# Kernel tuning notes

Hardware: AMD Instinct MI355X
Metric: run time of the kernel (lower is better)

The kernel has to match this reference:

```python
import jax, jax.numpy as jnp
import numpy as np
import math

B, S, D = 2, 2048, 2048
H = 16
DK = D // H


def build_rotary(dim, seq_len):
    inv_freq = 1.0 / (10000.0 ** (np.arange(0, dim, 2, dtype=np.float32) / dim))
    t = np.arange(seq_len, dtype=np.float32)
    freqs = np.einsum('i,j->ij', t, inv_freq)
    emb = np.concatenate([freqs, freqs], axis=-1)  # [S, dim]
    return jnp.asarray(np.cos(emb))[None, None], jnp.asarray(np.sin(emb))[None, None]


def rotate_half(x):
    x1, x2 = jnp.split(x, 2, axis=-1)
    return jnp.concatenate([-x2, x1], axis=-1)


def setup_inputs() -> dict:
    key = jax.random.key(0)
    ks = jax.random.split(key, 12)
    s = 1.0 / math.sqrt(D)
    inp = {
        'query': jax.random.normal(ks[0], (B, S, D), jnp.float32),
        'key': jax.random.normal(ks[1], (B, S, D), jnp.float32),
        'value': jax.random.normal(ks[2], (B, S, D), jnp.float32),
        'mask': jnp.tril(jnp.ones((S, S), bool))[None, None],  # causal [1,1,S,S]
        'wq': jax.random.uniform(ks[3], (D, D), jnp.float32, -s, s),
        'bq': jax.random.uniform(ks[4], (D,), jnp.float32, -s, s),
        'wk': jax.random.uniform(ks[5], (D, D), jnp.float32, -s, s),
        'bk': jax.random.uniform(ks[6], (D,), jnp.float32, -s, s),
        'wv': jax.random.uniform(ks[7], (D, D), jnp.float32, -s, s),
        'bv': jax.random.uniform(ks[8], (D,), jnp.float32, -s, s),
        'wo': jax.random.uniform(ks[9], (D, D), jnp.float32, -s, s),
        'bo': jax.random.uniform(ks[10], (D,), jnp.float32, -s, s),
    }
    return inp


def reference(query, key, value, mask, wq, bq, wk, bk, wv, bv, wo, bo):
    Bc, Sc, _ = query.shape
    # QKV projections -> [B, H, S, DK]
    def proj(x, w, b):
        return (x @ w.T + b).reshape(Bc, Sc, H, DK).transpose(0, 2, 1, 3)
    q = proj(query, wq, bq)
    k = proj(key, wk, bk)
    v = proj(value, wv, bv)
    # inline RoPE
    cos, sin = build_rotary(DK, Sc)
    cos = cos.astype(query.dtype)
    sin = sin.astype(query.dtype)
    q = q * cos + rotate_half(q) * sin
    k = k * cos + rotate_half(k) * sin
    # attention (dropout in eval / identity)
    scores = jnp.einsum('bhqd,bhkd->bhqk', q, k) / math.sqrt(DK)
    scores = jnp.where(mask, scores.astype(jnp.float32), -1e9)
    p = jax.nn.softmax(scores, axis=-1)
    x = jnp.einsum('bhqk,bhkd->bhqd', p, v)
    x = x.transpose(0, 2, 1, 3).reshape(Bc, Sc, H * DK)
    return x @ wo.T + bo
```

## Files before the change

### kernel.cpp

```cpp
#include <hip/hip_runtime.h>
#include <hip/hip_bf16.h>

#define Bc 2
#define Sc 2048
#define Dc 2048
#define Hc 16
#define DKc 128
#define Mc (Bc * Sc)
#define Kc Dc
#define Nc Dc
#define NX ((size_t)Bc * Sc * Dc)
#define NW ((size_t)Dc * Dc)

#define SM_C 0.1275174366f

typedef unsigned short u16;
using bf16x8  = __bf16 __attribute__((ext_vector_type(8)));
using ushort8 = unsigned short __attribute__((ext_vector_type(8)));
using ushort4v = unsigned short __attribute__((ext_vector_type(4)));
using floatx4 = float __attribute__((ext_vector_type(4)));
using float4v = float __attribute__((ext_vector_type(4)));

__device__ __forceinline__ u16 f2bf(float f) {
  union { float f; unsigned u; } x; x.f = f;
  unsigned r = x.u + 0x7fffu + ((x.u >> 16) & 1u);
  return (u16)(r >> 16);
}
__device__ __forceinline__ float bf2f(u16 u) {
  union { unsigned u; float f; } x; x.u = ((unsigned)u) << 16;
  return x.f;
}
__device__ __forceinline__ bf16x8 load8(const u16* p) {
  return __builtin_bit_cast(bf16x8, *(const ushort8*)p);
}
__device__ __forceinline__ floatx4 mfma16(bf16x8 a, bf16x8 b, floatx4 c) {
  return __builtin_amdgcn_mfma_f32_16x16x32_bf16(a, b, c, 0, 0, 0);
}
__device__ __forceinline__ void async16(const void* g, void* l) {
  __builtin_amdgcn_global_load_lds(
      (__attribute__((address_space(1))) void*)(g),
      (__attribute__((address_space(3))) void*)(l), 16, 0, 0);
}

__global__ __launch_bounds__(256) void cast_all(
    const float* __restrict__ q, const float* __restrict__ k,
    const float* __restrict__ v, const float* __restrict__ wq,
    const float* __restrict__ wk, const float* __restrict__ wv,
    const float* __restrict__ wo, u16* __restrict__ dst) {
  size_t i4 = (size_t)blockIdx.x * 256 + threadIdx.x;
  size_t e = i4 * 4;
  const float* src; size_t off;
  if (e < 3 * NX) {
    size_t w = e / NX;
    src = (w == 0) ? q : (w == 1) ? k : v;
    off = e - w * NX;
  } else {
    size_t e2 = e - 3 * NX;
    size_t w = e2 / NW;
    src = (w == 0) ? wq : (w == 1) ? wk : (w == 2) ? wv : wo;
    off = e2 - w * NW;
  }
  float4v val = *(const float4v*)(src + off);
  ushort4v o;
  o.x = f2bf(val.x); o.y = f2bf(val.y); o.z = f2bf(val.z); o.w = f2bf(val.w);
  *(ushort4v*)(dst + e) = o;
}

__device__ __forceinline__ void gemm_body(
    const u16* __restrict__ A, const u16* __restrict__ W,
    const float* __restrict__ bias, u16* __restrict__ out_bf,
    float* __restrict__ out_f, int epi, int m0, int n0, u16* Asl, u16* Bsl) {
  const int tid = threadIdx.x;
  const int wid = tid >> 6, lane = tid & 63;
  const int l15 = lane & 15, quad = lane >> 4;
  const int wm = wid & 1, wn = wid >> 1;

  floatx4 acc[4][4] = {};
  const int row_s = tid >> 2;
  const int col_s = (tid & 3) * 8;

  for (int k0 = 0; k0 < Kc; k0 += 32) {
    __syncthreads();
    const u16* ga0 = A + (size_t)(m0 + row_s) * Kc + k0 + col_s;
    const u16* gb0 = W + (size_t)(n0 + row_s) * Kc + k0 + col_s;
    async16(ga0, &Asl[tid * 8]);
    async16(ga0 + (size_t)64 * Kc, &Asl[2048 + tid * 8]);
    async16(gb0, &Bsl[tid * 8]);
    async16(gb0 + (size_t)64 * Kc, &Bsl[2048 + tid * 8]);
    __syncthreads();
    bf16x8 af[4], bfr[4];
#pragma unroll
    for (int i = 0; i < 4; i++)
      af[i] = load8(&Asl[(wm * 64 + i * 16 + l15) * 32 + quad * 8]);
#pragma unroll
    for (int j = 0; j < 4; j++)
      bfr[j] = load8(&Bsl[(wn * 64 + j * 16 + l15) * 32 + quad * 8]);
#pragma unroll
    for (int i = 0; i < 4; i++)
#pragma unroll
      for (int j = 0; j < 4; j++)
        acc[i][j] = mfma16(af[i], bfr[j], acc[i][j]);
  }

#pragma unroll
  for (int j = 0; j < 4; j++) {
    int col = n0 + wn * 64 + j * 16 + l15;
    float bv = bias[col];
#pragma unroll
    for (int i = 0; i < 4; i++) {
      int rowb = m0 + wm * 64 + i * 16 + quad * 4;
#pragma unroll
      for (int r = 0; r < 4; r++) {
        float v = acc[i][j][r] + bv;
        int row = rowb + r;
        if (epi == 2) {
          out_f[(size_t)row * Nc + col] = v;
        } else {
          int b = row >> 11, s = row & 2047;
          int h = col >> 7, dk = col & 127;
          size_t addr = (epi == 0)
              ? ((size_t)(b * Hc + h) * Sc + s) * DKc + dk
              : ((size_t)(b * Hc + h) * DKc + dk) * Sc + s;
          out_bf[addr] = f2bf(v);
        }
      }
    }
  }
}

__global__ __launch_bounds__(256, 2) void gemm_qkv(
    const u16* __restrict__ xq, const u16* __restrict__ xk,
    const u16* __restrict__ xv, const u16* __restrict__ wcat,
    const float* __restrict__ bq, const float* __restrict__ bk,
    const float* __restrict__ bv, u16* __restrict__ qhw,
    u16* __restrict__ khw, u16* __restrict__ vtw) {
  __shared__ u16 Asl[128 * 32];
  __shared__ u16 Bsl[128 * 32];
  const int proj = blockIdx.x >> 4;
  const int n0 = (blockIdx.x & 15) * 128;
  const int m0 = blockIdx.y * 128;
  const u16* A = (proj == 0) ? xq : (proj == 1) ? xk : xv;
  const u16* W = wcat + (size_t)proj * 2048 * Kc;
  const float* bias = (proj == 0) ? bq : (proj == 1) ? bk : bv;
  u16* outp = (proj == 0) ? qhw : (proj == 1) ? khw : vtw;
  gemm_body(A, W, bias, outp, nullptr, (proj == 2) ? 1 : 0, m0, n0, Asl, Bsl);
}

__global__ __launch_bounds__(256, 2) void gemm_out(
    const u16* __restrict__ A, const u16* __restrict__ W,
    const float* __restrict__ bias, float* __restrict__ out_f) {
  __shared__ u16 Asl[128 * 32];
  __shared__ u16 Bsl[128 * 32];
  gemm_body(A, W, bias, nullptr, out_f, 2, blockIdx.y * 128, blockIdx.x * 128,
            Asl, Bsl);
}

__global__ __launch_bounds__(256) void rope_kernel(u16* __restrict__ q,
                                                   u16* __restrict__ k) {
  int i = blockIdx.x * 256 + threadIdx.x;
  int d = i & 63;
  int s = (i >> 6) & (Sc - 1);
  int bh = i >> 17;
  size_t base = ((size_t)bh * Sc + s) * DKc;
  float inv_freq = exp2f((float)d * (-13.287712379549449f / 64.0f));
  float ang = (float)s * inv_freq;
  float sn, cs;
  sincosf(ang, &sn, &cs);
  float q1 = bf2f(q[base + d]), q2 = bf2f(q[base + d + 64]);
  q[base + d]      = f2bf((q1 * cs - q2 * sn) * SM_C);
  q[base + d + 64] = f2bf((q2 * cs + q1 * sn) * SM_C);
  float k1 = bf2f(k[base + d]), k2 = bf2f(k[base + d + 64]);
  k[base + d]      = f2bf(k1 * cs - k2 * sn);
  k[base + d + 64] = f2bf(k2 * cs + k1 * sn);
}

__global__ __launch_bounds__(256) void attn_kernel(
    const u16* __restrict__ qh, const u16* __restrict__ kh,
    const u16* __restrict__ vt, u16* __restrict__ ao) {
  __shared__ u16 Ksl[128 * 128];
  __shared__ u16 Vsl[144 * 128];
  const int tid = threadIdx.x;
  const int wid = tid >> 6, lane = tid & 63;
  const int l15 = lane & 15, quad = lane >> 4;
  const int qt = (blockIdx.z == 0) ? 15 - (int)blockIdx.x : (int)blockIdx.x;
  const int h = blockIdx.y, bb = blockIdx.z;
  const int bh = bb * Hc + h;
  const int q0 = qt * 128;
  const u16* qbase = qh + (size_t)bh * Sc * DKc;
  const u16* kbase = kh + (size_t)bh * Sc * DKc;
  const u16* vbase = vt + (size_t)bh * DKc * Sc;

  const int srow = tid >> 4;
  const int scol = (tid & 15) * 8;
  const int sdst = ((tid & 15) ^ srow) * 8;

  {
    int r = 128 + srow;
    u16 val = (r == 128) ? (u16)0x3F80 : (u16)0;
#pragma unroll
    for (int j = 0; j < 8; j++) Vsl[r * 128 + scol + j] = val;
  }

  bf16x8 qf[2][4];
#pragma unroll
  for (int mt = 0; mt < 2; mt++)
#pragma unroll
    for (int kq = 0; kq < 4; kq++)
      qf[mt][kq] = load8(qbase + (size_t)(q0 + wid * 32 + mt * 16 + l15) * DKc +
                         kq * 32 + quad * 8);

  floatx4 accO[2][9] = {};

  ushort8 kr[8], vr[8];
#pragma unroll
  for (int c = 0; c < 8; c++) {
    int rr = c * 16 + srow;
    kr[c] = *(const ushort8*)(kbase + (size_t)rr * DKc + scol);
    vr[c] = *(const ushort8*)(vbase + (size_t)rr * Sc + scol);
  }

  for (int kt = 0; kt <= qt; kt++) {
    __syncthreads();
#pragma unroll
    for (int c = 0; c < 8; c++) {
      int rr = c * 16 + srow;
      *(ushort8*)&Ksl[rr * 128 + sdst] = kr[c];
      *(ushort8*)&Vsl[rr * 128 + sdst] = vr[c];
    }
    __syncthreads();

    floatx4 sacc[2][8] = {};
#pragma unroll
    for (int kk = 0; kk < 4; kk++) {
      const int sb = ((kk * 4 + quad) ^ l15) * 8;
#pragma unroll
      for (int nt = 0; nt < 8; nt++) {
        bf16x8 kf = load8(&Ksl[(nt * 16 + l15) * 128 + sb]);
        sacc[0][nt] = mfma16(qf[0][kk], kf, sacc[0][nt]);
        sacc[1][nt] = mfma16(qf[1][kk], kf, sacc[1][nt]);
      }
    }

    if (kt == qt) {
#pragma unroll
      for (int nt = 0; nt < 8; nt++) {
        int kcol = nt * 16 + l15;
#pragma unroll
        for (int mt = 0; mt < 2; mt++) {
          int qrow = wid * 32 + mt * 16 + quad * 4;
#pragma unroll
          for (int r = 0; r < 4; r++)
            if (kcol > qrow + r) sacc[mt][nt][r] = -1e30f;
        }
      }
    }

#pragma unroll
    for (int mt = 0; mt < 2; mt++)
#pragma unroll
      for (int nt = 0; nt < 8; nt++)
#pragma unroll
        for (int r = 0; r < 4; r++)
          sacc[mt][nt][r] = exp2f(sacc[mt][nt][r]);

    __syncthreads();

    u16* Pw = &Ksl[wid * 4096];
#pragma unroll
    for (int mt = 0; mt < 2; mt++)
#pragma unroll
      for (int nt = 0; nt < 8; nt++)
#pragma unroll
        for (int r = 0; r < 4; r++) {
          int row = mt * 16 + quad * 4 + r;
          int col = nt * 16 + l15;
          int sb = (col >> 3) ^ (row & 15);
          Pw[row * 128 + sb * 8 + (col & 7)] = f2bf(sacc[mt][nt][r]);
        }

    if (kt < qt) {
      const u16* kb = kbase + (size_t)(kt + 1) * 128 * DKc;
#pragma unroll
      for (int c = 0; c < 8; c++) {
        int rr = c * 16 + srow;
        kr[c] = *(const ushort8*)(kb + (size_t)rr * DKc + scol);
        vr[c] = *(const ushort8*)(vbase + (size_t)rr * Sc + (kt + 1) * 128 + scol);
      }
    }

#pragma unroll
    for (int kk = 0; kk < 4; kk++) {
      const int sb = ((kk * 4 + quad) ^ l15) * 8;
      bf16x8 pf0 = load8(&Pw[(0 * 16 + l15) * 128 + sb]);
      bf16x8 pf1 = load8(&Pw[(1 * 16 + l15) * 128 + sb]);
#pragma unroll
      for (int nt = 0; nt < 9; nt++) {
        bf16x8 vf = load8(&Vsl[(nt * 16 + l15) * 128 + sb]);
        accO[0][nt] = mfma16(pf0, vf, accO[0][nt]);
        accO[1][nt] = mfma16(pf1, vf, accO[1][nt]);
      }
    }
  }

#pragma unroll
  for (int mt = 0; mt < 2; mt++)
#pragma unroll
    for (int r = 0; r < 4; r++) {
      float lsum = __shfl(accO[mt][8][r], lane & 48);
      float inv = 1.0f / lsum;
      int gq = q0 + wid * 32 + mt * 16 + quad * 4 + r;
      size_t rowbase = ((size_t)bb * Sc + gq) * Dc + h * DKc;
#pragma unroll
      for (int nt = 0; nt < 8; nt++)
        ao[rowbase + nt * 16 + l15] = f2bf(accO[mt][nt][r] * inv);
    }
}

extern "C" void kernel_launch(void* const* d_in, const int* in_sizes, int n_in,
                              void* d_out, int out_size, void* d_ws,
                              size_t ws_size, hipStream_t stream) {
  const float* q  = (const float*)d_in[0];
  const float* k  = (const float*)d_in[1];
  const float* v  = (const float*)d_in[2];
  const float* wq = (const float*)d_in[4];
  const float* bq = (const float*)d_in[5];
  const float* wk = (const float*)d_in[6];
  const float* bk = (const float*)d_in[7];
  const float* wv = (const float*)d_in[8];
  const float* bv = (const float*)d_in[9];
  const float* wo = (const float*)d_in[10];
  const float* bo = (const float*)d_in[11];
  float* out = (float*)d_out;

  u16* ws = (u16*)d_ws;
  u16* xq  = ws;
  u16* xk  = ws + NX;
  u16* xv  = ws + 2 * NX;
  u16* wcat = ws + 3 * NX;
  u16* wob = ws + 3 * NX + 3 * NW;
  u16* qhw = ws + 3 * NX + 4 * NW;
  u16* khw = ws + 4 * NX + 4 * NW;
  u16* vtw = ws + 5 * NX + 4 * NW;
  u16* aow = ws + 6 * NX + 4 * NW;

  {
    size_t tot4 = (3 * NX + 4 * NW) / 4;
    cast_all<<<dim3((unsigned)(tot4 / 256)), 256, 0, stream>>>(
        q, k, v, wq, wk, wv, wo, ws);
  }
  gemm_qkv<<<dim3(48, Mc / 128), 256, 0, stream>>>(
      xq, xk, xv, wcat, bq, bk, bv, qhw, khw, vtw);
  rope_kernel<<<dim3(Bc * Hc * Sc * 64 / 256), 256, 0, stream>>>(qhw, khw);
  attn_kernel<<<dim3(Sc / 128, Hc, Bc), 256, 0, stream>>>(qhw, khw, vtw, aow);
  gemm_out<<<dim3(Nc / 128, Mc / 128), 256, 0, stream>>>(aow, wob, bo, out);
}
```

Baseline: 533.2 us.

## Rewrite projection GEMMs as 256x256 tiles with 4-stage async LDS pipeline

```diff
diff --git a/kernel.cpp b/kernel.cpp
--- a/kernel.cpp
+++ b/kernel.cpp
@@ -11,6 +11,7 @@
 #define Nc Dc
 #define NX ((size_t)Bc * Sc * Dc)
 #define NW ((size_t)Dc * Dc)
+#define NTK (Kc / 32)
 
 #define SM_C 0.1275174366f
 
@@ -66,52 +67,96 @@
   *(ushort4v*)(dst + e) = o;
 }
 
-__device__ __forceinline__ void gemm_body(
+__device__ __forceinline__ void gemm256_body(
     const u16* __restrict__ A, const u16* __restrict__ W,
     const float* __restrict__ bias, u16* __restrict__ out_bf,
-    float* __restrict__ out_f, int epi, int m0, int n0, u16* Asl, u16* Bsl) {
+    float* __restrict__ out_f, int epi, int m0, int n0,
+    u16* __restrict__ lds ) {
   const int tid = threadIdx.x;
   const int wid = tid >> 6, lane = tid & 63;
   const int l15 = lane & 15, quad = lane >> 4;
-  const int wm = wid & 1, wn = wid >> 1;
-
-  floatx4 acc[4][4] = {};
-  const int row_s = tid >> 2;
-  const int col_s = (tid & 3) * 8;
-
-  for (int k0 = 0; k0 < Kc; k0 += 32) {
-    __syncthreads();
-    const u16* ga0 = A + (size_t)(m0 + row_s) * Kc + k0 + col_s;
-    const u16* gb0 = W + (size_t)(n0 + row_s) * Kc + k0 + col_s;
-    async16(ga0, &Asl[tid * 8]);
-    async16(ga0 + (size_t)64 * Kc, &Asl[2048 + tid * 8]);
-    async16(gb0, &Bsl[tid * 8]);
-    async16(gb0 + (size_t)64 * Kc, &Bsl[2048 + tid * 8]);
-    __syncthreads();
-    bf16x8 af[4], bfr[4];
-#pragma unroll
-    for (int i = 0; i < 4; i++)
-      af[i] = load8(&Asl[(wm * 64 + i * 16 + l15) * 32 + quad * 8]);
-#pragma unroll
-    for (int j = 0; j < 4; j++)
-      bfr[j] = load8(&Bsl[(wn * 64 + j * 16 + l15) * 32 + quad * 8]);
-#pragma unroll
-    for (int i = 0; i < 4; i++)
-#pragma unroll
-      for (int j = 0; j < 4; j++)
-        acc[i][j] = mfma16(af[i], bfr[j], acc[i][j]);
-  }
-
-#pragma unroll
-  for (int j = 0; j < 4; j++) {
-    int col = n0 + wn * 64 + j * 16 + l15;
+  const int wm = wid >> 2, wn = wid & 3;
+
+  const int sr = tid >> 2;
+  const int sc = (((tid & 3) ^ ((tid >> 3) & 3))) * 8;
+  const u16* gA = A + (size_t)(m0 + sr) * Kc + sc;
+  const u16* gB = W + (size_t)(n0 + sr) * Kc + sc;
+  const size_t rowskip = (size_t)128 * Kc;
+
+  const int slot8 = (quad ^ ((l15 >> 1) & 3)) * 8;
+  const int arow0 = (wm * 128 + l15) * 32 + slot8;
+  const int brow0 = (wn * 64 + l15) * 32 + slot8;
+
+  floatx4 acc[8][4] = {};
+
+#pragma unroll
+  for (int t = 0; t < 3; ++t) {
+    u16* buf = lds + t * 16384;
+    async16(gA + t * 32,           buf + tid * 8);
+    async16(gA + t * 32 + rowskip, buf + 4096 + tid * 8);
+    async16(gB + t * 32,           buf + 8192 + tid * 8);
+    async16(gB + t * 32 + rowskip, buf + 12288 + tid * 8);
+  }
+  asm volatile("s_waitcnt vmcnt(8)" ::: "memory");
+  __builtin_amdgcn_s_barrier();
+
+  for (int t = 0; t < NTK; ++t) {
+    u16* buf  = lds + (t & 3) * 16384;
+    u16* nbuf = lds + ((t + 3) & 3) * 16384;
+    const bool pf = (t + 3 < NTK);
+
+    if (pf) {
+      async16(gA + (t + 3) * 32,           nbuf + tid * 8);
+      async16(gA + (t + 3) * 32 + rowskip, nbuf + 4096 + tid * 8);
+    }
+    bf16x8 bfrag[4], afrag[4];
+#pragma unroll
+    for (int n = 0; n < 4; ++n)
+      bfrag[n] = load8(buf + 8192 + brow0 + n * 512);
+#pragma unroll
+    for (int m = 0; m < 4; ++m)
+      afrag[m] = load8(buf + arow0 + m * 512);
+    __builtin_amdgcn_s_barrier();
+    __builtin_amdgcn_s_setprio(1);
+#pragma unroll
+    for (int m = 0; m < 4; ++m)
+#pragma unroll
+      for (int n = 0; n < 4; ++n)
+        acc[m][n] = mfma16(afrag[m], bfrag[n], acc[m][n]);
+    __builtin_amdgcn_s_setprio(0);
+    __builtin_amdgcn_s_barrier();
+
+    if (pf) {
+      async16(gB + (t + 3) * 32,           nbuf + 8192 + tid * 8);
+      async16(gB + (t + 3) * 32 + rowskip, nbuf + 12288 + tid * 8);
+    }
+#pragma unroll
+    for (int m = 0; m < 4; ++m)
+      afrag[m] = load8(buf + arow0 + 2048 + m * 512);
+    __builtin_amdgcn_s_barrier();
+    __builtin_amdgcn_s_setprio(1);
+#pragma unroll
+    for (int m = 0; m < 4; ++m)
+#pragma unroll
+      for (int n = 0; n < 4; ++n)
+        acc[4 + m][n] = mfma16(afrag[m], bfrag[n], acc[4 + m][n]);
+    __builtin_amdgcn_s_setprio(0);
+    if (t < NTK - 3)       asm volatile("s_waitcnt vmcnt(8)" ::: "memory");
+    else if (t == NTK - 3) asm volatile("s_waitcnt vmcnt(4)" ::: "memory");
+    else                   asm volatile("s_waitcnt vmcnt(0)" ::: "memory");
+    __builtin_amdgcn_s_barrier();
+  }
+
+#pragma unroll
+  for (int n = 0; n < 4; ++n) {
+    int col = n0 + wn * 64 + n * 16 + l15;
     float bv = bias[col];
 #pragma unroll
-    for (int i = 0; i < 4; i++) {
-      int rowb = m0 + wm * 64 + i * 16 + quad * 4;
-#pragma unroll
-      for (int r = 0; r < 4; r++) {
-        float v = acc[i][j][r] + bv;
+    for (int mi = 0; mi < 8; ++mi) {
+      int rowb = m0 + wm * 128 + mi * 16 + quad * 4;
+#pragma unroll
+      for (int r = 0; r < 4; ++r) {
+        float v = acc[mi][n][r] + bv;
         int row = rowb + r;
         if (epi == 2) {
           out_f[(size_t)row * Nc + col] = v;
@@ -128,31 +173,29 @@
   }
 }
 
-__global__ __launch_bounds__(256, 2) void gemm_qkv(
+__global__ __launch_bounds__(512, 2) void gemm_qkv256(
     const u16* __restrict__ xq, const u16* __restrict__ xk,
     const u16* __restrict__ xv, const u16* __restrict__ wcat,
     const float* __restrict__ bq, const float* __restrict__ bk,
     const float* __restrict__ bv, u16* __restrict__ qhw,
     u16* __restrict__ khw, u16* __restrict__ vtw) {
-  __shared__ u16 Asl[128 * 32];
-  __shared__ u16 Bsl[128 * 32];
-  const int proj = blockIdx.x >> 4;
-  const int n0 = (blockIdx.x & 15) * 128;
-  const int m0 = blockIdx.y * 128;
+  __shared__ u16 lds[4 * 16384];
+  const int proj = blockIdx.z;
+  const int n0 = blockIdx.x * 256;
+  const int m0 = blockIdx.y * 256;
   const u16* A = (proj == 0) ? xq : (proj == 1) ? xk : xv;
   const u16* W = wcat + (size_t)proj * 2048 * Kc;
   const float* bias = (proj == 0) ? bq : (proj == 1) ? bk : bv;
   u16* outp = (proj == 0) ? qhw : (proj == 1) ? khw : vtw;
-  gemm_body(A, W, bias, outp, nullptr, (proj == 2) ? 1 : 0, m0, n0, Asl, Bsl);
-}
-
-__global__ __launch_bounds__(256, 2) void gemm_out(
+  gemm256_body(A, W, bias, outp, nullptr, (proj == 2) ? 1 : 0, m0, n0, lds);
+}
+
+__global__ __launch_bounds__(512, 2) void gemm_out256(
     const u16* __restrict__ A, const u16* __restrict__ W,
     const float* __restrict__ bias, float* __restrict__ out_f) {
-  __shared__ u16 Asl[128 * 32];
-  __shared__ u16 Bsl[128 * 32];
-  gemm_body(A, W, bias, nullptr, out_f, 2, blockIdx.y * 128, blockIdx.x * 128,
-            Asl, Bsl);
+  __shared__ u16 lds[4 * 16384];
+  gemm256_body(A, W, bias, nullptr, out_f, 2, blockIdx.y * 256,
+               blockIdx.x * 256, lds);
 }
 
 __global__ __launch_bounds__(256) void rope_kernel(u16* __restrict__ q,
@@ -348,9 +391,9 @@
     cast_all<<<dim3((unsigned)(tot4 / 256)), 256, 0, stream>>>(
         q, k, v, wq, wk, wv, wo, ws);
   }
-  gemm_qkv<<<dim3(48, Mc / 128), 256, 0, stream>>>(
+  gemm_qkv256<<<dim3(Nc / 256, Mc / 256, 3), 512, 0, stream>>>(
       xq, xk, xv, wcat, bq, bk, bv, qhw, khw, vtw);
   rope_kernel<<<dim3(Bc * Hc * Sc * 64 / 256), 256, 0, stream>>>(qhw, khw);
   attn_kernel<<<dim3(Sc / 128, Hc, Bc), 256, 0, stream>>>(qhw, khw, vtw, aow);
-  gemm_out<<<dim3(Nc / 128, Mc / 128), 256, 0, stream>>>(aow, wob, bo, out);
-}
+  gemm_out256<<<dim3(Nc / 256, Mc / 256), 512, 0, stream>>>(aow, wob, bo, out);
+}
```

Result: slower. 557.1 us (+4.5%).

## Triple-buffer GEMM LDS tiles with async prefetch and XOR swizzle

Applied to the files above, without the earlier changes.

```diff
diff --git a/kernel.cpp b/kernel.cpp
--- a/kernel.cpp
+++ b/kernel.cpp
@@ -11,6 +11,7 @@
 #define Nc Dc
 #define NX ((size_t)Bc * Sc * Dc)
 #define NW ((size_t)Dc * Dc)
+#define NTK (Kc / 32)
 
 #define SM_C 0.1275174366f
 
@@ -69,49 +70,83 @@
 __device__ __forceinline__ void gemm_body(
     const u16* __restrict__ A, const u16* __restrict__ W,
     const float* __restrict__ bias, u16* __restrict__ out_bf,
-    float* __restrict__ out_f, int epi, int m0, int n0, u16* Asl, u16* Bsl) {
+    float* __restrict__ out_f, int epi, int m0, int n0,
+    u16* __restrict__ lds ) {
   const int tid = threadIdx.x;
   const int wid = tid >> 6, lane = tid & 63;
   const int l15 = lane & 15, quad = lane >> 4;
-  const int wm = wid & 1, wn = wid >> 1;
+  const int wm = wid >> 1, wn = wid & 1;
+
+  const int sr = tid >> 2;
+  const int sc = ((tid & 3) ^ ((tid >> 3) & 3)) * 8;
+  const u16* gA = A + (size_t)(m0 + sr) * Kc + sc;
+  const u16* gB = W + (size_t)(n0 + sr) * Kc + sc;
+  const size_t half = (size_t)64 * Kc;
+
+  const int slot8 = (quad ^ ((l15 >> 1) & 3)) * 8;
+  const int arow0 = (wm * 64 + l15) * 32 + slot8;
+  const int brow0 = 4096 + (wn * 64 + l15) * 32 + slot8;
 
   floatx4 acc[4][4] = {};
-  const int row_s = tid >> 2;
-  const int col_s = (tid & 3) * 8;
-
-  for (int k0 = 0; k0 < Kc; k0 += 32) {
-    __syncthreads();
-    const u16* ga0 = A + (size_t)(m0 + row_s) * Kc + k0 + col_s;
-    const u16* gb0 = W + (size_t)(n0 + row_s) * Kc + k0 + col_s;
-    async16(ga0, &Asl[tid * 8]);
-    async16(ga0 + (size_t)64 * Kc, &Asl[2048 + tid * 8]);
-    async16(gb0, &Bsl[tid * 8]);
-    async16(gb0 + (size_t)64 * Kc, &Bsl[2048 + tid * 8]);
-    __syncthreads();
+
+  u16* b0 = lds;
+  u16* b1 = lds + 8192;
+  u16* b2 = lds + 16384;
+
+  async16(gA,             b0 + tid * 8);
+  async16(gA + half,      b0 + 2048 + tid * 8);
+  async16(gB,             b0 + 4096 + tid * 8);
+  async16(gB + half,      b0 + 6144 + tid * 8);
+  async16(gA + 32,        b1 + tid * 8);
+  async16(gA + 32 + half, b1 + 2048 + tid * 8);
+  async16(gB + 32,        b1 + 4096 + tid * 8);
+  async16(gB + 32 + half, b1 + 6144 + tid * 8);
+  asm volatile("s_waitcnt vmcnt(4)" ::: "memory");
+  __builtin_amdgcn_s_barrier();
+
+  const u16* gAt = gA + 64;
+  const u16* gBt = gB + 64;
+
+  for (int t = 0; t < NTK; ++t) {
+    if (t < NTK - 2) {
+      async16(gAt,        b2 + tid * 8);
+      async16(gAt + half, b2 + 2048 + tid * 8);
+      async16(gBt,        b2 + 4096 + tid * 8);
+      async16(gBt + half, b2 + 6144 + tid * 8);
+    }
+
     bf16x8 af[4], bfr[4];
 #pragma unroll
-    for (int i = 0; i < 4; i++)
-      af[i] = load8(&Asl[(wm * 64 + i * 16 + l15) * 32 + quad * 8]);
-#pragma unroll
-    for (int j = 0; j < 4; j++)
-      bfr[j] = load8(&Bsl[(wn * 64 + j * 16 + l15) * 32 + quad * 8]);
-#pragma unroll
-    for (int i = 0; i < 4; i++)
-#pragma unroll
-      for (int j = 0; j < 4; j++)
-        acc[i][j] = mfma16(af[i], bfr[j], acc[i][j]);
-  }
-
-#pragma unroll
-  for (int j = 0; j < 4; j++) {
-    int col = n0 + wn * 64 + j * 16 + l15;
+    for (int m = 0; m < 4; ++m) af[m] = load8(b0 + arow0 + m * 512);
+#pragma unroll
+    for (int n = 0; n < 4; ++n) bfr[n] = load8(b0 + brow0 + n * 512);
+
+    __builtin_amdgcn_s_setprio(1);
+#pragma unroll
+    for (int m = 0; m < 4; ++m)
+#pragma unroll
+      for (int n = 0; n < 4; ++n)
+        acc[m][n] = mfma16(af[m], bfr[n], acc[m][n]);
+    __builtin_amdgcn_s_setprio(0);
+
+    if (t < NTK - 2)       asm volatile("s_waitcnt vmcnt(4)" ::: "memory");
+    else if (t == NTK - 2) asm volatile("s_waitcnt vmcnt(0)" ::: "memory");
+    __builtin_amdgcn_s_barrier();
+
+    u16* tmp = b0; b0 = b1; b1 = b2; b2 = tmp;
+    gAt += 32; gBt += 32;
+  }
+
+#pragma unroll
+  for (int n = 0; n < 4; ++n) {
+    int col = n0 + wn * 64 + n * 16 + l15;
     float bv = bias[col];
 #pragma unroll
-    for (int i = 0; i < 4; i++) {
-      int rowb = m0 + wm * 64 + i * 16 + quad * 4;
-#pragma unroll
-      for (int r = 0; r < 4; r++) {
-        float v = acc[i][j][r] + bv;
+    for (int m = 0; m < 4; ++m) {
+      int rowb = m0 + wm * 64 + m * 16 + quad * 4;
+#pragma unroll
+      for (int r = 0; r < 4; ++r) {
+        float v = acc[m][n][r] + bv;
         int row = rowb + r;
         if (epi == 2) {
           out_f[(size_t)row * Nc + col] = v;
@@ -128,31 +163,29 @@
   }
 }
 
-__global__ __launch_bounds__(256, 2) void gemm_qkv(
+__global__ __launch_bounds__(256, 3) void gemm_qkv(
     const u16* __restrict__ xq, const u16* __restrict__ xk,
     const u16* __restrict__ xv, const u16* __restrict__ wcat,
     const float* __restrict__ bq, const float* __restrict__ bk,
     const float* __restrict__ bv, u16* __restrict__ qhw,
     u16* __restrict__ khw, u16* __restrict__ vtw) {
-  __shared__ u16 Asl[128 * 32];
-  __shared__ u16 Bsl[128 * 32];
-  const int proj = blockIdx.x >> 4;
-  const int n0 = (blockIdx.x & 15) * 128;
+  __shared__ u16 lds[3 * 8192];
+  const int proj = blockIdx.z;
+  const int n0 = blockIdx.x * 128;
   const int m0 = blockIdx.y * 128;
   const u16* A = (proj == 0) ? xq : (proj == 1) ? xk : xv;
   const u16* W = wcat + (size_t)proj * 2048 * Kc;
   const float* bias = (proj == 0) ? bq : (proj == 1) ? bk : bv;
   u16* outp = (proj == 0) ? qhw : (proj == 1) ? khw : vtw;
-  gemm_body(A, W, bias, outp, nullptr, (proj == 2) ? 1 : 0, m0, n0, Asl, Bsl);
-}
-
-__global__ __launch_bounds__(256, 2) void gemm_out(
+  gemm_body(A, W, bias, outp, nullptr, (proj == 2) ? 1 : 0, m0, n0, lds);
+}
+
+__global__ __launch_bounds__(256, 3) void gemm_out(
     const u16* __restrict__ A, const u16* __restrict__ W,
     const float* __restrict__ bias, float* __restrict__ out_f) {
-  __shared__ u16 Asl[128 * 32];
-  __shared__ u16 Bsl[128 * 32];
-  gemm_body(A, W, bias, nullptr, out_f, 2, blockIdx.y * 128, blockIdx.x * 128,
-            Asl, Bsl);
+  __shared__ u16 lds[3 * 8192];
+  gemm_body(A, W, bias, nullptr, out_f, 2, blockIdx.y * 128,
+            blockIdx.x * 128, lds);
 }
 
 __global__ __launch_bounds__(256) void rope_kernel(u16* __restrict__ q,
@@ -348,7 +381,7 @@
     cast_all<<<dim3((unsigned)(tot4 / 256)), 256, 0, stream>>>(
         q, k, v, wq, wk, wv, wo, ws);
   }
-  gemm_qkv<<<dim3(48, Mc / 128), 256, 0, stream>>>(
+  gemm_qkv<<<dim3(Nc / 128, Mc / 128, 3), 256, 0, stream>>>(
       xq, xk, xv, wcat, bq, bk, bv, qhw, khw, vtw);
   rope_kernel<<<dim3(Bc * Hc * Sc * 64 / 256), 256, 0, stream>>>(qhw, khw);
   attn_kernel<<<dim3(Sc / 128, Hc, Bc), 256, 0, stream>>>(qhw, khw, vtw, aow);
```

New measurement: 508.5 us. -4.6%, faster.
